# Kernel optimization log

Hardware: AMD Instinct MI355X
Metric: run time of the kernel (lower is better)

Reference implementation:

```python
import jax, jax.numpy as jnp
import numpy as np

T, HID, H, KV, D = 2048, 2048, 16, 8, 128
EPS = 1e-6
THETA = 10000.0


def setup_inputs() -> dict:
    key = jax.random.key(0)
    ks = jax.random.split(key, 6)
    positions = jnp.arange(T, dtype=jnp.int64 if jax.config.jax_enable_x64 else jnp.int32)
    hidden_states = jax.random.normal(ks[0], (T, HID), dtype=jnp.float32)
    scale = 0.02
    Wq = jax.random.normal(ks[1], (HID, H * 2 * D), dtype=jnp.float32) * scale
    Wk = jax.random.normal(ks[2], (HID, KV * D), dtype=jnp.float32) * scale
    Wv = jax.random.normal(ks[3], (HID, KV * D), dtype=jnp.float32) * scale
    Wo = jax.random.normal(ks[4], (H * D, HID), dtype=jnp.float32) * scale
    q_norm_w = jnp.zeros((D,), dtype=jnp.float32)  # torch init: zeros, applied as (1+w)
    k_norm_w = jnp.zeros((D,), dtype=jnp.float32)
    return {"positions": positions, "hidden_states": hidden_states, "Wq": Wq,
            "Wk": Wk, "Wv": Wv, "Wo": Wo, "q_norm_w": q_norm_w, "k_norm_w": k_norm_w}


def _rms_norm(x, w):
    # fp32 RMSNorm with (1 + weight) scaling, per last dim
    xf = x.astype(jnp.float32)
    inv = jax.lax.rsqrt(jnp.mean(xf * xf, axis=-1, keepdims=True) + EPS)
    return (xf * inv * (1.0 + w.astype(jnp.float32))).astype(x.dtype)


def _rope(x, positions):
    # neox-style rotary over full head_dim; x: (T, heads, D)
    half = D // 2
    inv_freq = 1.0 / (THETA ** (jnp.arange(0, half, dtype=jnp.float32) / half))
    freqs = positions.astype(jnp.float32)[:, None] * inv_freq  # (T, half)
    cos = jnp.cos(freqs)[:, None, :]  # (T,1,half)
    sin = jnp.sin(freqs)[:, None, :]
    x1, x2 = x[..., :half], x[..., half:]
    return jnp.concatenate([x1 * cos - x2 * sin, x2 * cos + x1 * sin], axis=-1)


def reference(positions, hidden_states, Wq, Wk, Wv, Wo, q_norm_w, k_norm_w):
    scaling = D ** -0.5
    qg = (hidden_states @ Wq).reshape(T, H, 2 * D)
    q, gate = qg[..., :D], qg[..., D:]              # (T,H,D) each
    k = (hidden_states @ Wk).reshape(T, KV, D)
    v = (hidden_states @ Wv).reshape(T, KV, D)
    q = _rms_norm(q, q_norm_w)
    k = _rms_norm(k, k_norm_w)
    q = _rope(q, positions)
    k = _rope(k, positions)
    # GQA: repeat kv heads
    rep = H // KV
    k = jnp.repeat(k, rep, axis=1)                   # (T,H,D)
    v = jnp.repeat(v, rep, axis=1)
    scores = jnp.einsum('thd,shd->hts', q, k) * scaling  # (H,T,T)
    causal = positions[:, None] >= positions[None, :]     # (T,T)
    scores = jnp.where(causal[None], scores, jnp.finfo(scores.dtype).min)
    probs = jax.nn.softmax(scores, axis=-1)
    o = jnp.einsum('hts,shd->thd', probs, v).reshape(T, H * D)
    o = o * jax.nn.sigmoid(gate.reshape(T, H * D))
    return o @ Wo
```

## Files before the change

### kernel.cpp

```cpp
#include <hip/hip_runtime.h>
#include <stdint.h>
#include <math.h>

#define T_SEQ 2048
#define HID   2048
#define NH    16
#define NKV   8
#define DH    128

typedef __bf16 bf16x8 __attribute__((ext_vector_type(8)));
typedef float  f32x4  __attribute__((ext_vector_type(4)));

__device__ __forceinline__ ushort f2bf(float f) {
  uint32_t u = __float_as_uint(f);
  u += 0x7FFF + ((u >> 16) & 1);
  return (ushort)(u >> 16);
}
__device__ __forceinline__ float bf2f(ushort u) {
  return __uint_as_float(((uint32_t)u) << 16);
}
__device__ __forceinline__ void gld16(const void* g, void* l) {
  __builtin_amdgcn_global_load_lds(
      (const __attribute__((address_space(1))) uint32_t*)g,
      (__attribute__((address_space(3))) uint32_t*)l, 16, 0, 0);
}

__global__ __launch_bounds__(256) void prep_kernel(
    const float* __restrict__ hs, const float* __restrict__ Wq,
    const float* __restrict__ Wk, const float* __restrict__ Wv,
    ushort* __restrict__ hs16, ushort* __restrict__ Wqt,
    ushort* __restrict__ Wkt, ushort* __restrict__ Wvt) {
  int bid = blockIdx.x;
  if (bid < 4096) {
    int i = (bid * 256 + threadIdx.x) * 4;
    float4 v = *(const float4*)(hs + i);
    ushort4 o = {f2bf(v.x), f2bf(v.y), f2bf(v.z), f2bf(v.w)};
    *(ushort4*)(hs16 + i) = o;
    return;
  }
  bid -= 4096;
  const float* src; ushort* dst; int N, bi, bj;
  if (bid < 8192)       { src = Wq; dst = Wqt; N = 4096; bj = bid & 127; bi = bid >> 7; }
  else if (bid < 10240) { bid -= 8192;  src = Wk; dst = Wkt; N = 1024; bj = bid & 31; bi = bid >> 5; }
  else                  { bid -= 10240; src = Wv; dst = Wvt; N = 1024; bj = bid & 31; bi = bid >> 5; }
  __shared__ float tile[32][33];
  int row = threadIdx.x >> 3, c4 = (threadIdx.x & 7) * 4;
  float4 v = *(const float4*)(src + (size_t)(bi * 32 + row) * N + bj * 32 + c4);
  tile[row][c4 + 0] = v.x; tile[row][c4 + 1] = v.y;
  tile[row][c4 + 2] = v.z; tile[row][c4 + 3] = v.w;
  __syncthreads();
  ushort4 o = {f2bf(tile[c4 + 0][row]), f2bf(tile[c4 + 1][row]),
               f2bf(tile[c4 + 2][row]), f2bf(tile[c4 + 3][row])};
  *(ushort4*)(dst + (size_t)(bj * 32 + row) * HID + bi * 32 + c4) = o;
}

__global__ __launch_bounds__(256) void prep_wo(const float* __restrict__ Wo,
                                               ushort* __restrict__ Wot) {
  int bid = blockIdx.x;
  int bj = bid & 63, bi = bid >> 6;
  __shared__ float tile[32][33];
  int row = threadIdx.x >> 3, c4 = (threadIdx.x & 7) * 4;
  float4 v = *(const float4*)(Wo + (size_t)(bi * 32 + row) * HID + bj * 32 + c4);
  tile[row][c4 + 0] = v.x; tile[row][c4 + 1] = v.y;
  tile[row][c4 + 2] = v.z; tile[row][c4 + 3] = v.w;
  __syncthreads();
  ushort4 o = {f2bf(tile[c4 + 0][row]), f2bf(tile[c4 + 1][row]),
               f2bf(tile[c4 + 2][row]), f2bf(tile[c4 + 3][row])};
  *(ushort4*)(Wot + (size_t)(bj * 32 + row) * HID + bi * 32 + c4) = o;
}

template <int OUT_BF16>
__device__ __forceinline__ void gemm_core(
    const ushort* __restrict__ A, const ushort* __restrict__ Bt,
    float* __restrict__ Cf, ushort* __restrict__ Cb, int N, int K,
    int m0, int n0, ushort* As, ushort* Bs) {
  const int tid = threadIdx.x, lane = tid & 63, w = tid >> 6;
  const int quad = lane >> 4, l15 = lane & 15;
  const int wm = (w >> 1) * 64, wn = (w & 1) * 64;
  f32x4 acc[4][4];
#pragma unroll
  for (int i = 0; i < 4; ++i)
#pragma unroll
    for (int j = 0; j < 4; ++j) acc[i][j] = (f32x4){0.f, 0.f, 0.f, 0.f};

  const int srow = tid >> 2, sch = tid & 3;
  for (int k0 = 0; k0 < K; k0 += 32) {
    __syncthreads();
#pragma unroll
    for (int p = 0; p < 2; ++p) {
      int row = p * 64 + srow;
      int gch = sch ^ ((row >> 1) & 3);
      gld16(A + (size_t)(m0 + row) * K + k0 + gch * 8,
            As + (p * 256 + w * 64) * 8);
      gld16(Bt + (size_t)(n0 + row) * K + k0 + gch * 8,
            Bs + (p * 256 + w * 64) * 8);
    }
    __syncthreads();
    bf16x8 af[4], bfr[4];
#pragma unroll
    for (int mi = 0; mi < 4; ++mi) {
      int row = wm + mi * 16 + l15;
      int pch = quad ^ ((row >> 1) & 3);
      af[mi] = *(const bf16x8*)(As + row * 32 + pch * 8);
    }
#pragma unroll
    for (int ni = 0; ni < 4; ++ni) {
      int row = wn + ni * 16 + l15;
      int pch = quad ^ ((row >> 1) & 3);
      bfr[ni] = *(const bf16x8*)(Bs + row * 32 + pch * 8);
    }
#pragma unroll
    for (int mi = 0; mi < 4; ++mi)
#pragma unroll
      for (int ni = 0; ni < 4; ++ni)
        acc[mi][ni] = __builtin_amdgcn_mfma_f32_16x16x32_bf16(
            af[mi], bfr[ni], acc[mi][ni], 0, 0, 0);
  }
#pragma unroll
  for (int mi = 0; mi < 4; ++mi)
#pragma unroll
    for (int ni = 0; ni < 4; ++ni)
#pragma unroll
      for (int r = 0; r < 4; ++r) {
        int row = m0 + wm + mi * 16 + quad * 4 + r;
        int col = n0 + wn + ni * 16 + l15;
        if (OUT_BF16) Cb[(size_t)row * N + col] = f2bf(acc[mi][ni][r]);
        else          Cf[(size_t)row * N + col] = acc[mi][ni][r];
      }
}

__global__ __launch_bounds__(256) void gemm_qkv(
    const ushort* __restrict__ hs16, const ushort* __restrict__ Wqt,
    const ushort* __restrict__ Wkt, const ushort* __restrict__ Wvt,
    ushort* __restrict__ qg16, ushort* __restrict__ kb16,
    ushort* __restrict__ v16t) {
  __shared__ ushort As[128 * 32];
  __shared__ ushort Bs[128 * 32];
  int b = blockIdx.x;
  if (b < 512) {
    gemm_core<1>(hs16, Wqt, nullptr, qg16, 4096, HID, (b >> 5) * 128,
                 (b & 31) * 128, As, Bs);
  } else if (b < 640) {
    int f = b - 512;
    gemm_core<1>(hs16, Wkt, nullptr, kb16, 1024, HID, (f >> 3) * 128,
                 (f & 7) * 128, As, Bs);
  } else {
    int f = b - 640;
    gemm_core<1>(Wvt, hs16, nullptr, v16t, 2048, HID, (f >> 4) * 128,
                 (f & 15) * 128, As, Bs);
  }
}

__global__ __launch_bounds__(256) void gemm_out(
    const ushort* __restrict__ ob16, const ushort* __restrict__ Wot,
    float* __restrict__ out) {
  __shared__ ushort As[128 * 32];
  __shared__ ushort Bs[128 * 32];
  int b = blockIdx.x;
  gemm_core<0>(ob16, Wot, out, nullptr, HID, HID, (b >> 4) * 128,
               (b & 15) * 128, As, Bs);
}

__global__ __launch_bounds__(128) void norm_rope(
    const ushort* __restrict__ qg16, const ushort* __restrict__ kb16,
    const int* __restrict__ positions, const float* __restrict__ qw,
    const float* __restrict__ kw, ushort* __restrict__ q16,
    ushort* __restrict__ k16) {
  const int t = blockIdx.x, hh = blockIdx.y, d = threadIdx.x;
  const ushort* x; const float* wgt; ushort* out;
  if (hh < NH) {
    x = qg16 + ((size_t)t * NH + hh) * (2 * DH); wgt = qw;
    out = q16 + ((size_t)t * NH + hh) * DH;
  } else {
    x = kb16 + ((size_t)t * NKV + (hh - NH)) * DH; wgt = kw;
    out = k16 + ((size_t)t * NKV + (hh - NH)) * DH;
  }
  float v = bf2f(x[d]);
  float ss = v * v;
#pragma unroll
  for (int off = 32; off >= 1; off >>= 1) ss += __shfl_xor(ss, off, 64);
  __shared__ float red[2];
  if ((d & 63) == 0) red[d >> 6] = ss;
  __syncthreads();
  float mean = (red[0] + red[1]) * (1.0f / 128.0f);
  float xn = v * rsqrtf(mean + 1e-6f) * (1.0f + wgt[d]);
  __shared__ float sh[128];
  sh[d] = xn;
  __syncthreads();
  if (d < 64) {
    float pos = (float)positions[t];
    float freq = pos * exp2f(-(float)d * (13.287712379549449f / 64.0f));
    float s, c;
    sincosf(freq, &s, &c);
    float x1 = sh[d], x2 = sh[d + 64];
    out[d]      = f2bf(x1 * c - x2 * s);
    out[d + 64] = f2bf(x2 * c + x1 * s);
  }
}

__global__ __launch_bounds__(256) void attn_mfma(
    const ushort* __restrict__ q16, const ushort* __restrict__ k16,
    const ushort* __restrict__ v16t, const float* __restrict__ qnw,
    const float* __restrict__ knw, ushort* __restrict__ Op0,
    ushort* __restrict__ Op1, float* __restrict__ lpart) {
  const int pb = blockIdx.x, h = blockIdx.y, s = blockIdx.z, kvh = h >> 1;
  const int tid = threadIdx.x, lane = tid & 63, w = tid >> 6;
  const int quad = lane >> 4, l15 = lane & 15;

  __shared__ ushort Ks[2][64 * 128];
  __shared__ ushort Vs[2][144 * 64];
  __shared__ ushort Ps[4][16][72];

#pragma unroll
  for (int buf = 0; buf < 2; ++buf)
    for (int i = tid; i < 16 * 64; i += 256) {
      int row = 128 + (i >> 6), col = i & 63;
      Vs[buf][row * 64 + col] = (row == 128) ? (ushort)0x3F80 : (ushort)0;
    }

  __shared__ float s8[8];
  __shared__ float bshare;
  {
    float mq = 0.f, mk = 0.f;
    if (tid < 128) { mq = fabsf(1.f + qnw[tid]); mk = fabsf(1.f + knw[tid]); }
#pragma unroll
    for (int off = 32; off >= 1; off >>= 1) {
      mq = fmaxf(mq, __shfl_xor(mq, off, 64));
      mk = fmaxf(mk, __shfl_xor(mk, off, 64));
    }
    if (lane == 0) { s8[w * 2] = mq; s8[w * 2 + 1] = mk; }
    __syncthreads();
    if (tid == 0) {
      float MQ = fmaxf(s8[0], s8[2]), MK = fmaxf(s8[1], s8[3]);
      bshare = 16.3217f * MQ * MK * 1.02f + 0.1f;
    }
    __syncthreads();
  }
  const float B = bshare;
  const float CSC = 0.08838834764831845f * 1.44269504088896f;

#pragma unroll 1
  for (int sel = 0; sel < 2; ++sel) {
    const int qt = sel ? (31 - pb) : pb;
    const int q0 = qt * 64, nk = qt + 1;
    const int ntl = (nk > s) ? ((nk - s + 1) >> 1) : 0;

    bf16x8 qf[4];
    const ushort* qbase = q16 + ((size_t)(q0 + w * 16 + l15) * NH + h) * DH;
#pragma unroll
    for (int ks = 0; ks < 4; ++ks)
      qf[ks] = *(const bf16x8*)(qbase + ks * 32 + quad * 8);

    f32x4 oacc[9];
#pragma unroll
    for (int i = 0; i < 9; ++i) oacc[i] = (f32x4){0.f, 0.f, 0.f, 0.f};

    __syncthreads();
    if (ntl > 0) {
      const int kt0 = s * 64;
#pragma unroll
      for (int p = 0; p < 4; ++p) {
        int row = p * 16 + (tid >> 4), ch = tid & 15;
        int gch = ch ^ (row & 15);
        gld16(k16 + ((size_t)(kt0 + row) * NKV + kvh) * DH + gch * 8,
              (ushort*)Ks[0] + (p * 256 + w * 64) * 8);
      }
#pragma unroll
      for (int p = 0; p < 4; ++p) {
        int row = p * 32 + (tid >> 3), ch = tid & 7;
        int gch = ch ^ (row & 7);
        gld16(v16t + (size_t)(kvh * DH + row) * T_SEQ + kt0 + gch * 8,
              (ushort*)Vs[0] + (p * 256 + w * 64) * 8);
      }
    }

#pragma unroll 1
    for (int it = 0; it < ntl; ++it) {
      const int kt = s + 2 * it;
      const int cur = it & 1;
      __syncthreads();
      if (it + 1 < ntl) {
        const int nt0 = (kt + 2) * 64;
#pragma unroll
        for (int p = 0; p < 4; ++p) {
          int row = p * 16 + (tid >> 4), ch = tid & 15;
          int gch = ch ^ (row & 15);
          gld16(k16 + ((size_t)(nt0 + row) * NKV + kvh) * DH + gch * 8,
                (ushort*)Ks[1 - cur] + (p * 256 + w * 64) * 8);
        }
#pragma unroll
        for (int p = 0; p < 4; ++p) {
          int row = p * 32 + (tid >> 3), ch = tid & 7;
          int gch = ch ^ (row & 7);
          gld16(v16t + (size_t)(kvh * DH + row) * T_SEQ + nt0 + gch * 8,
                (ushort*)Vs[1 - cur] + (p * 256 + w * 64) * 8);
        }
      }

      f32x4 sacc[4];
#pragma unroll
      for (int ni = 0; ni < 4; ++ni) sacc[ni] = (f32x4){0.f, 0.f, 0.f, 0.f};
      const ushort* KsC = Ks[cur];
#pragma unroll
      for (int ks = 0; ks < 4; ++ks)
#pragma unroll
        for (int ni = 0; ni < 4; ++ni) {
          int row = ni * 16 + l15;
          int pch = (ks * 4 + quad) ^ (row & 15);
          bf16x8 kf = *(const bf16x8*)(KsC + row * 128 + pch * 8);
          sacc[ni] = __builtin_amdgcn_mfma_f32_16x16x32_bf16(
              qf[ks], kf, sacc[ni], 0, 0, 0);
        }

      const bool diag = (kt == qt);
      const int kt0 = kt * 64;
#pragma unroll
      for (int ni = 0; ni < 4; ++ni) {
        int key = kt0 + ni * 16 + l15;
#pragma unroll
        for (int r = 0; r < 4; ++r) {
          float arg = fmaf(sacc[ni][r], CSC, -B);
          float pv;
          if (diag) {
            int q = q0 + w * 16 + quad * 4 + r;
            pv = (key <= q) ? exp2f(arg) : 0.f;
          } else {
            pv = exp2f(arg);
          }
          Ps[w][quad * 4 + r][ni * 16 + l15] = f2bf(pv);
        }
      }

      const ushort* VsC = Vs[cur];
#pragma unroll
      for (int ks2 = 0; ks2 < 2; ++ks2) {
        bf16x8 pf = *(const bf16x8*)(&Ps[w][l15][ks2 * 32 + quad * 8]);
#pragma unroll
        for (int ni = 0; ni < 9; ++ni) {
          int row = ni * 16 + l15;
          int pch = (ks2 * 4 + quad) ^ (row & 7);
          bf16x8 vf = *(const bf16x8*)(VsC + row * 64 + pch * 8);
          oacc[ni] = __builtin_amdgcn_mfma_f32_16x16x32_bf16(
              pf, vf, oacc[ni], 0, 0, 0);
        }
      }
    }

    ushort* Op = s ? Op1 : Op0;
#pragma unroll
    for (int ni = 0; ni < 8; ++ni) {
      int d = ni * 16 + l15;
#pragma unroll
      for (int r = 0; r < 4; ++r) {
        int q = q0 + w * 16 + quad * 4 + r;
        Op[((size_t)h * T_SEQ + q) * DH + d] = f2bf(oacc[ni][r]);
      }
    }
    if (l15 == 0) {
#pragma unroll
      for (int r = 0; r < 4; ++r) {
        int q = q0 + w * 16 + quad * 4 + r;
        lpart[(size_t)s * (NH * T_SEQ) + h * T_SEQ + q] = oacc[8][r];
      }
    }
  }
}

__global__ __launch_bounds__(256) void combine_kernel(
    const ushort* __restrict__ Op0, const ushort* __restrict__ Op1,
    const float* __restrict__ lpart, const ushort* __restrict__ qg16,
    ushort* __restrict__ ob16) {
  const int t = blockIdx.x, tid = threadIdx.x;
  const int h = tid >> 4, d0 = (tid & 15) * 8;
  const float l = lpart[h * T_SEQ + t] + lpart[NH * T_SEQ + h * T_SEQ + t];
  const float inv = 1.0f / l;
  const size_t po = ((size_t)h * T_SEQ + t) * DH + d0;
  ushort4 a0 = *(const ushort4*)(Op0 + po);
  ushort4 a1 = *(const ushort4*)(Op0 + po + 4);
  ushort4 b0 = *(const ushort4*)(Op1 + po);
  ushort4 b1 = *(const ushort4*)(Op1 + po + 4);
  const ushort* gp = qg16 + ((size_t)t * NH + h) * (2 * DH) + DH + d0;
  ushort4 g0 = *(const ushort4*)(gp);
  ushort4 g1 = *(const ushort4*)(gp + 4);
  float oa[8] = {bf2f(a0.x), bf2f(a0.y), bf2f(a0.z), bf2f(a0.w),
                 bf2f(a1.x), bf2f(a1.y), bf2f(a1.z), bf2f(a1.w)};
  float ob[8] = {bf2f(b0.x), bf2f(b0.y), bf2f(b0.z), bf2f(b0.w),
                 bf2f(b1.x), bf2f(b1.y), bf2f(b1.z), bf2f(b1.w)};
  float gg[8] = {bf2f(g0.x), bf2f(g0.y), bf2f(g0.z), bf2f(g0.w),
                 bf2f(g1.x), bf2f(g1.y), bf2f(g1.z), bf2f(g1.w)};
  ushort r[8];
#pragma unroll
  for (int i = 0; i < 8; ++i) {
    float o = (oa[i] + ob[i]) * inv;
    o = o / (1.0f + exp2f(-gg[i] * 1.44269504088896f));
    r[i] = f2bf(o);
  }
  ushort* op = ob16 + (size_t)t * (NH * DH) + h * DH + d0;
  *(ushort4*)(op)     = (ushort4){r[0], r[1], r[2], r[3]};
  *(ushort4*)(op + 4) = (ushort4){r[4], r[5], r[6], r[7]};
}

extern "C" void kernel_launch(void* const* d_in, const int* in_sizes, int n_in,
                              void* d_out, int out_size, void* d_ws, size_t ws_size,
                              hipStream_t stream) {
  const int*   positions = (const int*)d_in[0];
  const float* hs  = (const float*)d_in[1];
  const float* Wq  = (const float*)d_in[2];
  const float* Wk  = (const float*)d_in[3];
  const float* Wv  = (const float*)d_in[4];
  const float* Wo  = (const float*)d_in[5];
  const float* qnw = (const float*)d_in[6];
  const float* knw = (const float*)d_in[7];
  float* out = (float*)d_out;

  const size_t MB = 1 << 20;
  uint8_t* ws = (uint8_t*)d_ws;
  ushort* qg16 = (ushort*)(ws + 0);
  ushort* Op0  = (ushort*)(ws + 16 * MB);
  ushort* kb16 = (ushort*)(ws + 16 * MB);
  ushort* hs16 = (ushort*)(ws + 20 * MB);
  float*  lpart= (float*)(ws + 24 * MB);
  ushort* Wqt  = (ushort*)(ws + 28 * MB);
  ushort* q16  = (ushort*)(ws + 28 * MB);
  ushort* Wot  = (ushort*)(ws + 36 * MB);
  ushort* Wkt  = (ushort*)(ws + 44 * MB);
  ushort* k16  = (ushort*)(ws + 44 * MB);
  ushort* Wvt  = (ushort*)(ws + 48 * MB);
  ushort* ob16 = (ushort*)(ws + 48 * MB);
  ushort* v16t = (ushort*)(ws + 52 * MB);
  ushort* Op1  = (ushort*)(ws + 56 * MB);

  prep_kernel<<<16384, 256, 0, stream>>>(hs, Wq, Wk, Wv, hs16, Wqt, Wkt, Wvt);
  gemm_qkv<<<768, 256, 0, stream>>>(hs16, Wqt, Wkt, Wvt, qg16, kb16, v16t);
  norm_rope<<<dim3(T_SEQ, NH + NKV), 128, 0, stream>>>(qg16, kb16, positions,
                                                       qnw, knw, q16, k16);
  prep_wo<<<4096, 256, 0, stream>>>(Wo, Wot);
  attn_mfma<<<dim3(16, NH, 2), 256, 0, stream>>>(q16, k16, v16t, qnw, knw,
                                                 Op0, Op1, lpart);
  combine_kernel<<<T_SEQ, 256, 0, stream>>>(Op0, Op1, lpart, qg16, ob16);
  gemm_out<<<256, 256, 0, stream>>>(ob16, Wot, out);
}
```

Before: 301.4 us.

## Fuse QK RMSNorm+RoPE into QKV GEMM epilogue, merge Wo prep, retile out GEMM

Moves the per-head RMSNorm and rotary embedding into the QKV GEMM epilogue, so the separate norm_rope kernel and its round trip of the qg/k intermediates through memory go away. The gate half is now written to its own buffer. The Wo transpose/convert is folded into the single prep launch, and the output GEMM uses 64-row tiles to launch twice as many blocks. Probabilities feeding P·V are truncated to bf16 instead of rounded, and the epilogue uses hardware sin/cos on range-reduced inputs, which trades a little accuracy for fewer instructions.

```diff
diff --git a/kernel.cpp b/kernel.cpp
--- a/kernel.cpp
+++ b/kernel.cpp
@@ -16,6 +16,9 @@
   u += 0x7FFF + ((u >> 16) & 1);
   return (ushort)(u >> 16);
 }
+__device__ __forceinline__ ushort f2bf_rz(float f) {
+  return (ushort)(__float_as_uint(f) >> 16);
+}
 __device__ __forceinline__ float bf2f(ushort u) {
   return __uint_as_float(((uint32_t)u) << 16);
 }
@@ -28,8 +31,10 @@
 __global__ __launch_bounds__(256) void prep_kernel(
     const float* __restrict__ hs, const float* __restrict__ Wq,
     const float* __restrict__ Wk, const float* __restrict__ Wv,
-    ushort* __restrict__ hs16, ushort* __restrict__ Wqt,
-    ushort* __restrict__ Wkt, ushort* __restrict__ Wvt) {
+    const float* __restrict__ Wo, ushort* __restrict__ hs16,
+    ushort* __restrict__ Wqt, ushort* __restrict__ Wkt,
+    ushort* __restrict__ Wvt, ushort* __restrict__ Wot) {
+  __shared__ float tile[32][33];
   int bid = blockIdx.x;
   if (bid < 4096) {
     int i = (bid * 256 + threadIdx.x) * 4;
@@ -42,8 +47,8 @@
   const float* src; ushort* dst; int N, bi, bj;
   if (bid < 8192)       { src = Wq; dst = Wqt; N = 4096; bj = bid & 127; bi = bid >> 7; }
   else if (bid < 10240) { bid -= 8192;  src = Wk; dst = Wkt; N = 1024; bj = bid & 31; bi = bid >> 5; }
-  else                  { bid -= 10240; src = Wv; dst = Wvt; N = 1024; bj = bid & 31; bi = bid >> 5; }
-  __shared__ float tile[32][33];
+  else if (bid < 12288) { bid -= 10240; src = Wv; dst = Wvt; N = 1024; bj = bid & 31; bi = bid >> 5; }
+  else                  { bid -= 12288; src = Wo; dst = Wot; N = 2048; bj = bid & 63; bi = bid >> 6; }
   int row = threadIdx.x >> 3, c4 = (threadIdx.x & 7) * 4;
   float4 v = *(const float4*)(src + (size_t)(bi * 32 + row) * N + bj * 32 + c4);
   tile[row][c4 + 0] = v.x; tile[row][c4 + 1] = v.y;
@@ -54,51 +59,34 @@
   *(ushort4*)(dst + (size_t)(bj * 32 + row) * HID + bi * 32 + c4) = o;
 }
 
-__global__ __launch_bounds__(256) void prep_wo(const float* __restrict__ Wo,
-                                               ushort* __restrict__ Wot) {
-  int bid = blockIdx.x;
-  int bj = bid & 63, bi = bid >> 6;
-  __shared__ float tile[32][33];
-  int row = threadIdx.x >> 3, c4 = (threadIdx.x & 7) * 4;
-  float4 v = *(const float4*)(Wo + (size_t)(bi * 32 + row) * HID + bj * 32 + c4);
-  tile[row][c4 + 0] = v.x; tile[row][c4 + 1] = v.y;
-  tile[row][c4 + 2] = v.z; tile[row][c4 + 3] = v.w;
-  __syncthreads();
-  ushort4 o = {f2bf(tile[c4 + 0][row]), f2bf(tile[c4 + 1][row]),
-               f2bf(tile[c4 + 2][row]), f2bf(tile[c4 + 3][row])};
-  *(ushort4*)(Wot + (size_t)(bj * 32 + row) * HID + bi * 32 + c4) = o;
-}
-
-template <int OUT_BF16>
-__device__ __forceinline__ void gemm_core(
+template <int MI>
+__device__ __forceinline__ void gemm_loop(
     const ushort* __restrict__ A, const ushort* __restrict__ Bt,
-    float* __restrict__ Cf, ushort* __restrict__ Cb, int N, int K,
-    int m0, int n0, ushort* As, ushort* Bs) {
+    int K, int m0, int n0, ushort* As, ushort* Bs, f32x4 (*acc)[4]) {
   const int tid = threadIdx.x, lane = tid & 63, w = tid >> 6;
   const int quad = lane >> 4, l15 = lane & 15;
-  const int wm = (w >> 1) * 64, wn = (w & 1) * 64;
-  f32x4 acc[4][4];
-#pragma unroll
-  for (int i = 0; i < 4; ++i)
-#pragma unroll
-    for (int j = 0; j < 4; ++j) acc[i][j] = (f32x4){0.f, 0.f, 0.f, 0.f};
-
+  const int wm = (w >> 1) * (MI * 16), wn = (w & 1) * 64;
   const int srow = tid >> 2, sch = tid & 3;
   for (int k0 = 0; k0 < K; k0 += 32) {
     __syncthreads();
 #pragma unroll
-    for (int p = 0; p < 2; ++p) {
+    for (int p = 0; p < MI / 2; ++p) {
       int row = p * 64 + srow;
       int gch = sch ^ ((row >> 1) & 3);
       gld16(A + (size_t)(m0 + row) * K + k0 + gch * 8,
             As + (p * 256 + w * 64) * 8);
+    }
+#pragma unroll
+    for (int p = 0; p < 2; ++p) {
+      int row = p * 64 + srow;
+      int gch = sch ^ ((row >> 1) & 3);
       gld16(Bt + (size_t)(n0 + row) * K + k0 + gch * 8,
             Bs + (p * 256 + w * 64) * 8);
     }
     __syncthreads();
-    bf16x8 af[4], bfr[4];
-#pragma unroll
-    for (int mi = 0; mi < 4; ++mi) {
+    bf16x8 af[MI], bfr[4];
+#pragma unroll
+    for (int mi = 0; mi < MI; ++mi) {
       int row = wm + mi * 16 + l15;
       int pch = quad ^ ((row >> 1) & 3);
       af[mi] = *(const bf16x8*)(As + row * 32 + pch * 8);
@@ -110,12 +98,20 @@
       bfr[ni] = *(const bf16x8*)(Bs + row * 32 + pch * 8);
     }
 #pragma unroll
-    for (int mi = 0; mi < 4; ++mi)
+    for (int mi = 0; mi < MI; ++mi)
 #pragma unroll
       for (int ni = 0; ni < 4; ++ni)
         acc[mi][ni] = __builtin_amdgcn_mfma_f32_16x16x32_bf16(
             af[mi], bfr[ni], acc[mi][ni], 0, 0, 0);
   }
+}
+
+__device__ __forceinline__ void bf16_store(f32x4 (*acc)[4],
+                                           ushort* __restrict__ Cb, int Ncols,
+                                           int m0, int n0) {
+  const int lane = threadIdx.x & 63, w = threadIdx.x >> 6;
+  const int quad = lane >> 4, l15 = lane & 15;
+  const int wm = (w >> 1) * 64, wn = (w & 1) * 64;
 #pragma unroll
   for (int mi = 0; mi < 4; ++mi)
 #pragma unroll
@@ -124,78 +120,138 @@
       for (int r = 0; r < 4; ++r) {
         int row = m0 + wm + mi * 16 + quad * 4 + r;
         int col = n0 + wn + ni * 16 + l15;
-        if (OUT_BF16) Cb[(size_t)row * N + col] = f2bf(acc[mi][ni][r]);
-        else          Cf[(size_t)row * N + col] = acc[mi][ni][r];
-      }
+        Cb[(size_t)row * Ncols + col] = f2bf(acc[mi][ni][r]);
+      }
+}
+
+__device__ __forceinline__ void norm_rope_epilogue(
+    f32x4 (*acc)[4], const float* __restrict__ wgt,
+    const int* __restrict__ positions, int m0, ushort* __restrict__ outp,
+    int ostride, char* smem) {
+  ushort* tile = (ushort*)smem;
+  float* ssum = (float*)(smem + 34816);
+  const int tid = threadIdx.x, lane = tid & 63, w = tid >> 6;
+  const int quad = lane >> 4, l15 = lane & 15;
+  const int wm = (w >> 1) * 64, wn = (w & 1) * 64;
+  float sp[4][4];
+#pragma unroll
+  for (int mi = 0; mi < 4; ++mi)
+#pragma unroll
+    for (int r = 0; r < 4; ++r) {
+      float s = 0.f;
+#pragma unroll
+      for (int ni = 0; ni < 4; ++ni) { float v = acc[mi][ni][r]; s += v * v; }
+#pragma unroll
+      for (int off = 1; off <= 8; off <<= 1) s += __shfl_xor(s, off, 64);
+      sp[mi][r] = s;
+    }
+  if (l15 == 0) {
+#pragma unroll
+    for (int mi = 0; mi < 4; ++mi)
+#pragma unroll
+      for (int r = 0; r < 4; ++r)
+        ssum[(w & 1) * 128 + wm + mi * 16 + quad * 4 + r] = sp[mi][r];
+  }
+  __syncthreads();
+  float wv[4];
+#pragma unroll
+  for (int ni = 0; ni < 4; ++ni) wv[ni] = 1.f + wgt[wn + ni * 16 + l15];
+#pragma unroll
+  for (int mi = 0; mi < 4; ++mi)
+#pragma unroll
+    for (int r = 0; r < 4; ++r) {
+      int row = wm + mi * 16 + quad * 4 + r;
+      float inv = rsqrtf((ssum[row] + ssum[128 + row]) * (1.f / 128.f) + 1e-6f);
+#pragma unroll
+      for (int ni = 0; ni < 4; ++ni)
+        tile[row * 136 + wn + ni * 16 + l15] =
+            f2bf(acc[mi][ni][r] * inv * wv[ni]);
+    }
+  __syncthreads();
+  const int row = tid >> 1, d0 = (tid & 1) * 32;
+  const float pos = (float)positions[m0 + row];
+  __align__(16) ushort lo[32], hi[32];
+#pragma unroll
+  for (int j = 0; j < 32; ++j) {
+    int d = d0 + j;
+    float rev = pos * exp2f((float)d * -0.20762050593045233f) *
+                0.15915494309189535f;
+    float fr = rev - floorf(rev);
+    float s = __builtin_amdgcn_sinf(fr);
+    float c = __builtin_amdgcn_cosf(fr);
+    float x1 = bf2f(tile[row * 136 + d]);
+    float x2 = bf2f(tile[row * 136 + d + 64]);
+    lo[j] = f2bf(x1 * c - x2 * s);
+    hi[j] = f2bf(x2 * c + x1 * s);
+  }
+  ushort* op = outp + (size_t)(m0 + row) * ostride + d0;
+#pragma unroll
+  for (int j = 0; j < 4; ++j) {
+    *((uint4*)op + j)        = ((const uint4*)lo)[j];
+    *((uint4*)(op + 64) + j) = ((const uint4*)hi)[j];
+  }
 }
 
 __global__ __launch_bounds__(256) void gemm_qkv(
     const ushort* __restrict__ hs16, const ushort* __restrict__ Wqt,
     const ushort* __restrict__ Wkt, const ushort* __restrict__ Wvt,
-    ushort* __restrict__ qg16, ushort* __restrict__ kb16,
+    const int* __restrict__ positions, const float* __restrict__ qnw,
+    const float* __restrict__ knw, ushort* __restrict__ q16,
+    ushort* __restrict__ gate16, ushort* __restrict__ k16,
     ushort* __restrict__ v16t) {
-  __shared__ ushort As[128 * 32];
-  __shared__ ushort Bs[128 * 32];
-  int b = blockIdx.x;
+  __shared__ __align__(16) char smem[35840 + 1024];
+  ushort* As = (ushort*)smem;
+  ushort* Bs = As + 4096;
+  f32x4 acc[4][4];
+#pragma unroll
+  for (int i = 0; i < 4; ++i)
+#pragma unroll
+    for (int j = 0; j < 4; ++j) acc[i][j] = (f32x4){0.f, 0.f, 0.f, 0.f};
+  const int b = blockIdx.x;
   if (b < 512) {
-    gemm_core<1>(hs16, Wqt, nullptr, qg16, 4096, HID, (b >> 5) * 128,
-                 (b & 31) * 128, As, Bs);
+    int mt = b >> 5, nt = b & 31, m0 = mt * 128, h = nt >> 1;
+    gemm_loop<4>(hs16, Wqt, HID, m0, nt * 128, As, Bs, acc);
+    if ((nt & 1) == 0)
+      norm_rope_epilogue(acc, qnw, positions, m0, q16 + h * DH, NH * DH, smem);
+    else
+      bf16_store(acc, gate16, NH * DH, m0, h * DH);
   } else if (b < 640) {
-    int f = b - 512;
-    gemm_core<1>(hs16, Wkt, nullptr, kb16, 1024, HID, (f >> 3) * 128,
-                 (f & 7) * 128, As, Bs);
+    int f = b - 512, mt = f >> 3, nt = f & 7, m0 = mt * 128;
+    gemm_loop<4>(hs16, Wkt, HID, m0, nt * 128, As, Bs, acc);
+    norm_rope_epilogue(acc, knw, positions, m0, k16 + nt * DH, NKV * DH, smem);
   } else {
-    int f = b - 640;
-    gemm_core<1>(Wvt, hs16, nullptr, v16t, 2048, HID, (f >> 4) * 128,
-                 (f & 15) * 128, As, Bs);
+    int f = b - 640, mt = f >> 4, nt = f & 15;
+    gemm_loop<4>(Wvt, hs16, HID, mt * 128, nt * 128, As, Bs, acc);
+    bf16_store(acc, v16t, T_SEQ, mt * 128, nt * 128);
   }
 }
 
 __global__ __launch_bounds__(256) void gemm_out(
     const ushort* __restrict__ ob16, const ushort* __restrict__ Wot,
     float* __restrict__ out) {
-  __shared__ ushort As[128 * 32];
+  __shared__ ushort As[64 * 32];
   __shared__ ushort Bs[128 * 32];
-  int b = blockIdx.x;
-  gemm_core<0>(ob16, Wot, out, nullptr, HID, HID, (b >> 4) * 128,
-               (b & 15) * 128, As, Bs);
-}
-
-__global__ __launch_bounds__(128) void norm_rope(
-    const ushort* __restrict__ qg16, const ushort* __restrict__ kb16,
-    const int* __restrict__ positions, const float* __restrict__ qw,
-    const float* __restrict__ kw, ushort* __restrict__ q16,
-    ushort* __restrict__ k16) {
-  const int t = blockIdx.x, hh = blockIdx.y, d = threadIdx.x;
-  const ushort* x; const float* wgt; ushort* out;
-  if (hh < NH) {
-    x = qg16 + ((size_t)t * NH + hh) * (2 * DH); wgt = qw;
-    out = q16 + ((size_t)t * NH + hh) * DH;
-  } else {
-    x = kb16 + ((size_t)t * NKV + (hh - NH)) * DH; wgt = kw;
-    out = k16 + ((size_t)t * NKV + (hh - NH)) * DH;
-  }
-  float v = bf2f(x[d]);
-  float ss = v * v;
-#pragma unroll
-  for (int off = 32; off >= 1; off >>= 1) ss += __shfl_xor(ss, off, 64);
-  __shared__ float red[2];
-  if ((d & 63) == 0) red[d >> 6] = ss;
-  __syncthreads();
-  float mean = (red[0] + red[1]) * (1.0f / 128.0f);
-  float xn = v * rsqrtf(mean + 1e-6f) * (1.0f + wgt[d]);
-  __shared__ float sh[128];
-  sh[d] = xn;
-  __syncthreads();
-  if (d < 64) {
-    float pos = (float)positions[t];
-    float freq = pos * exp2f(-(float)d * (13.287712379549449f / 64.0f));
-    float s, c;
-    sincosf(freq, &s, &c);
-    float x1 = sh[d], x2 = sh[d + 64];
-    out[d]      = f2bf(x1 * c - x2 * s);
-    out[d + 64] = f2bf(x2 * c + x1 * s);
-  }
+  f32x4 acc[2][4];
+#pragma unroll
+  for (int i = 0; i < 2; ++i)
+#pragma unroll
+    for (int j = 0; j < 4; ++j) acc[i][j] = (f32x4){0.f, 0.f, 0.f, 0.f};
+  const int b = blockIdx.x;
+  const int m0 = (b >> 4) * 64, n0 = (b & 15) * 128;
+  gemm_loop<2>(ob16, Wot, HID, m0, n0, As, Bs, acc);
+  const int lane = threadIdx.x & 63, w = threadIdx.x >> 6;
+  const int quad = lane >> 4, l15 = lane & 15;
+  const int wm = (w >> 1) * 32, wn = (w & 1) * 64;
+#pragma unroll
+  for (int mi = 0; mi < 2; ++mi)
+#pragma unroll
+    for (int ni = 0; ni < 4; ++ni)
+#pragma unroll
+      for (int r = 0; r < 4; ++r) {
+        int row = m0 + wm + mi * 16 + quad * 4 + r;
+        int col = n0 + wn + ni * 16 + l15;
+        out[(size_t)row * HID + col] = acc[mi][ni][r];
+      }
 }
 
 __global__ __launch_bounds__(256) void attn_mfma(
@@ -327,7 +383,7 @@
           } else {
             pv = exp2f(arg);
           }
-          Ps[w][quad * 4 + r][ni * 16 + l15] = f2bf(pv);
+          Ps[w][quad * 4 + r][ni * 16 + l15] = f2bf_rz(pv);
         }
       }
 
@@ -368,7 +424,7 @@
 
 __global__ __launch_bounds__(256) void combine_kernel(
     const ushort* __restrict__ Op0, const ushort* __restrict__ Op1,
-    const float* __restrict__ lpart, const ushort* __restrict__ qg16,
+    const float* __restrict__ lpart, const ushort* __restrict__ gate16,
     ushort* __restrict__ ob16) {
   const int t = blockIdx.x, tid = threadIdx.x;
   const int h = tid >> 4, d0 = (tid & 15) * 8;
@@ -379,7 +435,7 @@
   ushort4 a1 = *(const ushort4*)(Op0 + po + 4);
   ushort4 b0 = *(const ushort4*)(Op1 + po);
   ushort4 b1 = *(const ushort4*)(Op1 + po + 4);
-  const ushort* gp = qg16 + ((size_t)t * NH + h) * (2 * DH) + DH + d0;
+  const ushort* gp = gate16 + (size_t)t * (NH * DH) + h * DH + d0;
   ushort4 g0 = *(const ushort4*)(gp);
   ushort4 g1 = *(const ushort4*)(gp + 4);
   float oa[8] = {bf2f(a0.x), bf2f(a0.y), bf2f(a0.z), bf2f(a0.w),
@@ -415,28 +471,26 @@
 
   const size_t MB = 1 << 20;
   uint8_t* ws = (uint8_t*)d_ws;
-  ushort* qg16 = (ushort*)(ws + 0);
-  ushort* Op0  = (ushort*)(ws + 16 * MB);
-  ushort* kb16 = (ushort*)(ws + 16 * MB);
-  ushort* hs16 = (ushort*)(ws + 20 * MB);
-  float*  lpart= (float*)(ws + 24 * MB);
-  ushort* Wqt  = (ushort*)(ws + 28 * MB);
-  ushort* q16  = (ushort*)(ws + 28 * MB);
-  ushort* Wot  = (ushort*)(ws + 36 * MB);
-  ushort* Wkt  = (ushort*)(ws + 44 * MB);
-  ushort* k16  = (ushort*)(ws + 44 * MB);
-  ushort* Wvt  = (ushort*)(ws + 48 * MB);
-  ushort* ob16 = (ushort*)(ws + 48 * MB);
-  ushort* v16t = (ushort*)(ws + 52 * MB);
-  ushort* Op1  = (ushort*)(ws + 56 * MB);
-
-  prep_kernel<<<16384, 256, 0, stream>>>(hs, Wq, Wk, Wv, hs16, Wqt, Wkt, Wvt);
-  gemm_qkv<<<768, 256, 0, stream>>>(hs16, Wqt, Wkt, Wvt, qg16, kb16, v16t);
-  norm_rope<<<dim3(T_SEQ, NH + NKV), 128, 0, stream>>>(qg16, kb16, positions,
-                                                       qnw, knw, q16, k16);
-  prep_wo<<<4096, 256, 0, stream>>>(Wo, Wot);
+  ushort* hs16  = (ushort*)(ws + 0);
+  ushort* Op0   = (ushort*)(ws + 0);
+  ushort* Wqt   = (ushort*)(ws + 8 * MB);
+  ushort* Op1   = (ushort*)(ws + 8 * MB);
+  ushort* ob16  = (ushort*)(ws + 16 * MB);
+  ushort* Wkt   = (ushort*)(ws + 24 * MB);
+  float*  lpart = (float*)(ws + 24 * MB);
+  ushort* Wvt   = (ushort*)(ws + 28 * MB);
+  ushort* gate16= (ushort*)(ws + 32 * MB);
+  ushort* q16   = (ushort*)(ws + 40 * MB);
+  ushort* k16   = (ushort*)(ws + 48 * MB);
+  ushort* v16t  = (ushort*)(ws + 52 * MB);
+  ushort* Wot   = (ushort*)(ws + 56 * MB);
+
+  prep_kernel<<<20480, 256, 0, stream>>>(hs, Wq, Wk, Wv, Wo,
+                                         hs16, Wqt, Wkt, Wvt, Wot);
+  gemm_qkv<<<768, 256, 0, stream>>>(hs16, Wqt, Wkt, Wvt, positions, qnw, knw,
+                                    q16, gate16, k16, v16t);
   attn_mfma<<<dim3(16, NH, 2), 256, 0, stream>>>(q16, k16, v16t, qnw, knw,
                                                  Op0, Op1, lpart);
-  combine_kernel<<<T_SEQ, 256, 0, stream>>>(Op0, Op1, lpart, qg16, ob16);
-  gemm_out<<<256, 256, 0, stream>>>(ob16, Wot, out);
-}
+  combine_kernel<<<T_SEQ, 256, 0, stream>>>(Op0, Op1, lpart, gate16, ob16);
+  gemm_out<<<512, 256, 0, stream>>>(ob16, Wot, out);
+}
```

Result: no change. 297.5 us (-1.3%).
